# Performance work log

Measured on AMD Instinct MI355X. Metric: run time of the kernel, lower is better.

The kernel has to match this reference:

```python
import jax, jax.numpy as jnp
import numpy as np

# Fixed-shape Conformer chunked attention (Gemma3n audio style)
S = 8192          # seq_len
H = 16            # num_heads
D = 128           # head_dim
HD = H * D        # hidden size = 2048
C = 12            # chunk_size
MP = 12           # max_past_horizon
MF = 0            # max_future_horizon
CTX = C + MP + MF # context_size = 24
POS = MP + MF + 1 # pos_length = 13
N = (S + C - 1) // C            # num_blocks
PAD = N * C - S                 # pad_amount
Q_SCALE = D ** -0.5 * 1.4426950408889634  # head_dim**-0.5 / softplus(0)
SOFTCAP = 50.0


def setup_inputs() -> dict:
    key = jax.random.key(0)
    ks = jax.random.split(key, 8)
    w = lambda k, shape: jax.random.normal(k, shape, jnp.float32) * 0.02
    return {
        "hidden_states": jax.random.normal(ks[0], (1, S, HD), jnp.float32),
        "position_embeddings": jax.random.normal(ks[1], (POS, HD), jnp.float32),
        "Wq": w(ks[2], (HD, HD)),
        "Wk": w(ks[3], (HD, HD)),
        "Wv": w(ks[4], (HD, HD)),
        "W_rel": w(ks[5], (HD, HD)),
        "W_post": w(ks[6], (HD, HD)),
        "per_dim_scale": jax.random.normal(ks[7], (D,), jnp.float32) * 0.1,
    }


def reference(hidden_states, position_embeddings, Wq, Wk, Wv, W_rel, W_post, per_dim_scale):
    x = hidden_states[0]  # [S, HD]
    q = (x @ Wq).reshape(S, H, D) * (Q_SCALE * jax.nn.softplus(per_dim_scale))
    k = (x @ Wk).reshape(S, H, D)  # k_scale = 1.0
    v = (x @ Wv).reshape(S, H, D)

    # query blocks [N, C, H, D]
    qb = jnp.pad(q, ((0, PAD), (0, 0), (0, 0))).reshape(N, C, H, D)
    # key/value padded then gathered into sliding context blocks [N, CTX, H, D]
    kp = jnp.pad(k, ((MP, MF + C - 1), (0, 0), (0, 0)))
    vp = jnp.pad(v, ((MP, MF + C - 1), (0, 0), (0, 0)))
    idx = jnp.arange(N)[:, None] * C + jnp.arange(CTX)[None, :]  # [N, CTX]
    kb = kp[idx]
    vb = vp[idx]

    rel_k = (position_embeddings @ W_rel).reshape(POS, H, D)

    # content scores [H, N, C, CTX]
    ac = jnp.einsum('nchd,nkhd->hnck', qb, kb)
    # relative-position scores via shift trick
    bd = jnp.einsum('nchd,phd->hncp', qb, rel_k)          # [H, N, C, POS]
    bd = jnp.pad(bd, ((0, 0), (0, 0), (0, 0), (0, CTX + 1 - POS)))
    bd = bd.reshape(H, N, C * (CTX + 1))[:, :, :C * CTX].reshape(H, N, C, CTX)

    attn = jnp.tanh((ac + bd) / SOFTCAP) * SOFTCAP        # softcap
    attn = jax.nn.softmax(attn, axis=-1)

    out = jnp.einsum('hnck,nkhd->nchd', attn, vb).reshape(N * C, HD)[:S]
    return (out @ W_post)[None]  # [1, S, HD]
```

## Files before the change

kernel.cpp:

```cpp
#include <hip/hip_runtime.h>
#include <hip/hip_bf16.h>

#define S_LEN 8192
#define NH    16
#define HD    128
#define HID   2048
#define NQKV  6144
#define CHUNK 12
#define MP    12
#define CTX   24
#define POS   13
#define NBLK  683

typedef short bf16x8 __attribute__((ext_vector_type(8)));
typedef float f32x4  __attribute__((ext_vector_type(4)));
typedef unsigned short u16;
typedef u16 u16x8 __attribute__((ext_vector_type(8)));
typedef u16 u16x4 __attribute__((ext_vector_type(4)));

#define MFMA16 __builtin_amdgcn_mfma_f32_16x16x32_bf16

__device__ __forceinline__ void glds16(const u16* g, u16* l) {
  __builtin_amdgcn_global_load_lds(
      (__attribute__((address_space(1))) void*)(void*)g,
      (__attribute__((address_space(3))) void*)l, 16, 0, 0);
}

__device__ __forceinline__ u16 f2b(float f) {
  __hip_bfloat16 h = __float2bfloat16(f);
  return *(u16*)&h;
}

__global__ __launch_bounds__(256) void f32_to_bf16(const float* __restrict__ in,
                                                   u16* __restrict__ out, int n) {
  int i = (blockIdx.x * 256 + threadIdx.x) * 4;
  if (i < n) {
    float4 v = *(const float4*)(in + i);
    u16x4 o = {f2b(v.x), f2b(v.y), f2b(v.z), f2b(v.w)};
    *(u16x4*)(out + i) = o;
  }
}

__global__ __launch_bounds__(256) void transpose4(const float* __restrict__ W0,
                                                  const float* __restrict__ W1,
                                                  const float* __restrict__ W2,
                                                  const float* __restrict__ W3,
                                                  u16* __restrict__ out) {
  __shared__ u16 t[64][72];
  const int z = blockIdx.z;
  const float* in = (z == 0) ? W0 : (z == 1) ? W1 : (z == 2) ? W2 : W3;
  u16* dst = out + (size_t)z * HID * HID;
  const int bx = blockIdx.x * 64, by = blockIdx.y * 64;
  const int x = threadIdx.x & 63;
  const int y4 = threadIdx.x >> 6;
  for (int r = y4; r < 64; r += 4)
    t[r][x] = f2b(in[(size_t)(by + r) * HID + bx + x]);
  __syncthreads();
  for (int r = y4; r < 64; r += 4)
    dst[(size_t)(bx + r) * HID + by + x] = t[x][r];
}

__global__ void qscale_kernel(const float* __restrict__ pds, float* __restrict__ qs) {
  int d = threadIdx.x;
  float x = pds[d];
  float sp = log1pf(expf(x));
  qs[d] = 0.08838834764831845f * 1.4426950408889634f * sp;
}

__global__ __launch_bounds__(256) void relk_atomic(const float* __restrict__ pos,
                                                   const float* __restrict__ Wrel,
                                                   float* __restrict__ RELF) {
  const int col = blockIdx.x * 256 + threadIdx.x;
  const int c0 = blockIdx.y * 256;
  float acc[POS] = {};
  for (int c = c0; c < c0 + 256; ++c) {
    float wv = Wrel[(size_t)c * HID + col];
#pragma unroll
    for (int p = 0; p < POS; ++p) acc[p] += pos[p * HID + c] * wv;
  }
#pragma unroll
  for (int p = 0; p < POS; ++p) atomicAdd(&RELF[p * HID + col], acc[p]);
}

__global__ __launch_bounds__(256) void relk_cvt(const float* __restrict__ RELF,
                                                u16* __restrict__ REL) {
  int i = blockIdx.x * 256 + threadIdx.x;
  if (i < POS * HID) REL[i] = f2b(RELF[i]);
}

#define BMT 256
#define BNT 256
#define BKT 32
#define NT  (HID / BKT)

__global__ __launch_bounds__(512, 2) void gemm_bt(const u16* __restrict__ A,
                                                  const u16* __restrict__ Bt,
                                                  u16* __restrict__ Co,
                                                  float* __restrict__ Cf,
                                                  const float* __restrict__ colscale,
                                                  int NN, int csLimit) {
  __shared__ u16 lds[4][2][BMT * BKT];
  const int tid = threadIdx.x;
  const int lane = tid & 63, w = tid >> 6;
  const int quad = lane >> 4, l = lane & 15;
  const int wm = (w >> 2) * 128, wn = (w & 3) * 64;

  const int orig = blockIdx.y * gridDim.x + blockIdx.x;
  const int xcd = orig & 7, k = orig >> 3;
  const int bm = (xcd * 4 + (k & 3)) * BMT;
  const int bn = (k >> 2) * BNT;

  const int rdoff = (l >> 1) * 64 + (((((l & 1) << 2) | quad)) ^ ((l >> 1) & 7)) * 8;

  const int sl = (lane & 7) ^ (lane >> 3);
  const int srow = ((lane >> 3) << 1) + (sl >> 2);
  const int sk = (sl & 3) * 8;
  const u16* Ag0 = A + (size_t)(bm + w * 32 + srow) * HID + sk;
  const u16* Ag1 = Ag0 + (size_t)16 * HID;
  const u16* Bg0 = Bt + (size_t)(bn + w * 32 + srow) * HID + sk;
  const u16* Bg1 = Bg0 + (size_t)16 * HID;

  f32x4 acc[8][4] = {};

#pragma unroll
  for (int pt = 0; pt < 3; ++pt) {
    u16* sA = &lds[pt][0][w * 1024];
    u16* sB = &lds[pt][1][w * 1024];
    glds16(Ag0 + pt * BKT, sA);
    glds16(Ag1 + pt * BKT, sA + 512);
    glds16(Bg0 + pt * BKT, sB);
    glds16(Bg1 + pt * BKT, sB + 512);
  }
  asm volatile("s_waitcnt vmcnt(8)" ::: "memory");
  __builtin_amdgcn_s_barrier();

  bf16x8 afC[4], bfC[4], afN[4], bfN[4];
#pragma unroll
  for (int i = 0; i < 4; ++i)
    afC[i] = *(const bf16x8*)(&lds[0][0][0] + (wm + i * 16) * 32 + rdoff);
#pragma unroll
  for (int j = 0; j < 4; ++j)
    bfC[j] = *(const bf16x8*)(&lds[0][1][0] + (wn + j * 16) * 32 + rdoff);

#pragma unroll 1
  for (int t = 0; t < NT; ++t) {
    const u16* bufA = &lds[t & 3][0][0];
    u16* stA = &lds[(t + 3) & 3][0][w * 1024];
    u16* stB = &lds[(t + 3) & 3][1][w * 1024];
    const int kt = (t + 3) * BKT;
    const bool doStage = (t < NT - 3);

    if (doStage) {
      glds16(Ag0 + kt, stA);
      glds16(Ag1 + kt, stA + 512);
    }
    bf16x8 af1[4];
#pragma unroll
    for (int i = 0; i < 4; ++i)
      af1[i] = *(const bf16x8*)(bufA + (wm + 64 + i * 16) * 32 + rdoff);
    asm volatile("s_waitcnt lgkmcnt(4)" ::: "memory");
    __builtin_amdgcn_sched_barrier(0);
    __builtin_amdgcn_s_setprio(1);
#pragma unroll
    for (int i = 0; i < 4; ++i)
#pragma unroll
      for (int j = 0; j < 4; ++j)
        acc[i][j] = MFMA16(afC[i], bfC[j], acc[i][j], 0, 0, 0);
    __builtin_amdgcn_s_setprio(0);

    if (doStage) {
      glds16(Bg0 + kt, stB);
      glds16(Bg1 + kt, stB + 512);
    }
    asm volatile("s_waitcnt lgkmcnt(0)" ::: "memory");
    if (t < NT - 3)       asm volatile("s_waitcnt vmcnt(8)" ::: "memory");
    else if (t == NT - 3) asm volatile("s_waitcnt vmcnt(4)" ::: "memory");
    else if (t == NT - 2) asm volatile("s_waitcnt vmcnt(0)" ::: "memory");
    __builtin_amdgcn_sched_barrier(0);
    if (t < NT - 1) {
      __builtin_amdgcn_s_barrier();
      const u16* nA = &lds[(t + 1) & 3][0][0];
      const u16* nB = &lds[(t + 1) & 3][1][0];
#pragma unroll
      for (int i = 0; i < 4; ++i)
        afN[i] = *(const bf16x8*)(nA + (wm + i * 16) * 32 + rdoff);
#pragma unroll
      for (int j = 0; j < 4; ++j)
        bfN[j] = *(const bf16x8*)(nB + (wn + j * 16) * 32 + rdoff);
    }
    __builtin_amdgcn_s_setprio(1);
#pragma unroll
    for (int i = 0; i < 4; ++i)
#pragma unroll
      for (int j = 0; j < 4; ++j)
        acc[4 + i][j] = MFMA16(af1[i], bfC[j], acc[4 + i][j], 0, 0, 0);
    __builtin_amdgcn_s_setprio(0);
#pragma unroll
    for (int r = 0; r < 4; ++r) {
      afC[r] = afN[r];
      bfC[r] = bfN[r];
    }
  }

#pragma unroll
  for (int i = 0; i < 8; ++i)
#pragma unroll
    for (int j = 0; j < 4; ++j)
#pragma unroll
      for (int r = 0; r < 4; ++r) {
        int row = bm + wm + i * 16 + quad * 4 + r;
        int col = bn + wn + j * 16 + l;
        float v = acc[i][j][r];
        if (colscale && col < csLimit) v *= colscale[col & (HD - 1)];
        if (Cf) Cf[(size_t)row * NN + col] = v;
        else    Co[(size_t)row * NN + col] = f2b(v);
      }
}

__global__ __launch_bounds__(64) void attn_kernel(const u16* __restrict__ qkv,
                                                  const u16* __restrict__ relg,
                                                  u16* __restrict__ og) {
  __shared__ char smem[13824];
  u16* qs = (u16*)smem;
  u16* ks = (u16*)(smem + 4352);
  u16* vt = (u16*)smem;
  u16* ps = (u16*)(smem + 12288);
  const int n = blockIdx.x, h = blockIdx.y;
  const int lane = threadIdx.x;
  const int quad = lane >> 4, l = lane & 15;
  const int base = n * CHUNK;
  const u16x8 zero8 = {0, 0, 0, 0, 0, 0, 0, 0};

  const u16* qg = qkv + h * HD;
  const u16* kg = qkv + 2048 + h * HD;
  const u16* vg = qkv + 4096 + h * HD;

  u16x8 vld[8];
#pragma unroll
  for (int i = 0; i < 8; ++i) {
    int id = lane + 64 * i;
    int ctx = id & 31, dc = id >> 5;
    int s = base + ctx - MP;
    vld[i] = (ctx < CTX && s >= 0 && s < S_LEN)
                 ? *(const u16x8*)(vg + (size_t)s * NQKV + dc * 8)
                 : zero8;
  }

#pragma unroll
  for (int i = 0; i < 4; ++i) {
    int id = lane + 64 * i;
    int c = id >> 4, dc = id & 15;
    int s = base + c;
    u16x8 v = (c < CHUNK && s < S_LEN)
                  ? *(const u16x8*)(qg + (size_t)s * NQKV + dc * 8)
                  : zero8;
    *(u16x8*)(qs + c * 136 + dc * 8) = v;
  }
#pragma unroll
  for (int i = 0; i < 8; ++i) {
    int id = lane + 64 * i;
    int ctx = id >> 4, dc = id & 15;
    int s = base + ctx - MP;
    u16x8 v = (ctx < CTX && s >= 0 && s < S_LEN)
                  ? *(const u16x8*)(kg + (size_t)s * NQKV + dc * 8)
                  : zero8;
    *(u16x8*)(ks + ctx * 136 + dc * 8) = v;
  }
  __syncthreads();

  f32x4 ac0 = {0, 0, 0, 0}, ac1 = {0, 0, 0, 0}, bd = {0, 0, 0, 0};
#pragma unroll
  for (int t = 0; t < 4; ++t) {
    int d0 = t * 32;
    bf16x8 aQ = *(const bf16x8*)(qs + l * 136 + d0 + quad * 8);
    bf16x8 bK0 = *(const bf16x8*)(ks + l * 136 + d0 + quad * 8);
    bf16x8 bK1 = *(const bf16x8*)(ks + (16 + l) * 136 + d0 + quad * 8);
    bf16x8 bR = {0, 0, 0, 0, 0, 0, 0, 0};
    if (l < POS)
      bR = *(const bf16x8*)(relg + (size_t)l * HID + h * HD + d0 + quad * 8);
    ac0 = MFMA16(aQ, bK0, ac0, 0, 0, 0);
    ac1 = MFMA16(aQ, bK1, ac1, 0, 0, 0);
    bd = MFMA16(aQ, bR, bd, 0, 0, 0);
  }

  float p0[4], p1[4];
#pragma unroll
  for (int r = 0; r < 4; ++r) {
    int c = quad * 4 + r;
    int pi0 = l - c;
    int pi1 = 16 + l - c;
    int sp0 = pi0 < 0 ? 0 : (pi0 > 15 ? 15 : pi0);
    int sp1 = pi1 < 0 ? 0 : (pi1 > 15 ? 15 : pi1);
    float b0 = __shfl(bd[r], quad * 16 + sp0, 64);
    float b1 = __shfl(bd[r], quad * 16 + sp1, 64);
    b0 = (pi0 >= 0 && pi0 < POS) ? b0 : 0.0f;
    b1 = (pi1 >= 0 && pi1 < POS) ? b1 : 0.0f;
    float s0 = tanhf((ac0[r] + b0) * (1.0f / 50.0f)) * 50.0f;
    float s1 = tanhf((ac1[r] + b1) * (1.0f / 50.0f)) * 50.0f;
    bool v1 = (l < (CTX - 16));
    if (!v1) s1 = -1e30f;
    float mx = fmaxf(s0, s1);
#pragma unroll
    for (int d = 1; d < 16; d <<= 1) mx = fmaxf(mx, __shfl_xor(mx, d, 64));
    float e0 = __expf(s0 - mx);
    float e1 = v1 ? __expf(s1 - mx) : 0.0f;
    float sm = e0 + e1;
#pragma unroll
    for (int d = 1; d < 16; d <<= 1) sm += __shfl_xor(sm, d, 64);
    float inv = 1.0f / sm;
    p0[r] = e0 * inv;
    p1[r] = e1 * inv;
  }
  __syncthreads();

#pragma unroll
  for (int i = 0; i < 8; ++i) {
    int id = lane + 64 * i;
    int ctx = id & 31, dc = id >> 5;
#pragma unroll
    for (int jj = 0; jj < 8; ++jj) vt[(dc * 8 + jj) * 48 + ctx] = vld[i][jj];
  }
#pragma unroll
  for (int r = 0; r < 4; ++r) {
    int c = quad * 4 + r;
    ps[c * 48 + l] = f2b(p0[r]);
    ps[c * 48 + 16 + l] = f2b(p1[r]);
  }
  __syncthreads();

  bf16x8 aP = *(const bf16x8*)(ps + l * 48 + quad * 8);
#pragma unroll
  for (int nt = 0; nt < 8; ++nt) {
    bf16x8 bV = *(const bf16x8*)(vt + (nt * 16 + l) * 48 + quad * 8);
    f32x4 o = {0, 0, 0, 0};
    o = MFMA16(aP, bV, o, 0, 0, 0);
#pragma unroll
    for (int r = 0; r < 4; ++r) {
      int c = quad * 4 + r;
      int s = base + c;
      if (c < CHUNK && s < S_LEN)
        og[(size_t)s * HID + h * HD + nt * 16 + l] = f2b(o[r]);
    }
  }
}

extern "C" void kernel_launch(void* const* d_in, const int* in_sizes, int n_in,
                              void* d_out, int out_size, void* d_ws, size_t ws_size,
                              hipStream_t stream) {
  const float* x = (const float*)d_in[0];
  const float* pos = (const float*)d_in[1];
  const float* Wq = (const float*)d_in[2];
  const float* Wk = (const float*)d_in[3];
  const float* Wv = (const float*)d_in[4];
  const float* Wrel = (const float*)d_in[5];
  const float* Wpost = (const float*)d_in[6];
  const float* pds = (const float*)d_in[7];

  char* ws = (char*)d_ws;
  u16* WT  = (u16*)(ws);
  u16* xb  = (u16*)(ws + 33554432);
  u16* AO  = xb;
  u16* QKV = (u16*)(ws + 67108864);
  float* RELF = (float*)(ws + 167772160);
  u16* REL = (u16*)(ws + 167878656);
  float* QS = (float*)(ws + 167931904);

  const int NX = S_LEN * HID;
  f32_to_bf16<<<NX / 4 / 256, 256, 0, stream>>>(x, xb, NX);

  transpose4<<<dim3(32, 32, 4), 256, 0, stream>>>(Wq, Wk, Wv, Wpost, WT);
  qscale_kernel<<<1, 128, 0, stream>>>(pds, QS);

  hipMemsetAsync(RELF, 0, POS * HID * sizeof(float), stream);
  relk_atomic<<<dim3(8, 8), 256, 0, stream>>>(pos, Wrel, RELF);
  relk_cvt<<<(POS * HID + 255) / 256, 256, 0, stream>>>(RELF, REL);

  gemm_bt<<<dim3(32, 24), 512, 0, stream>>>(xb, WT, QKV, nullptr, QS, NQKV, 2048);

  attn_kernel<<<dim3(NBLK, NH), 64, 0, stream>>>(QKV, REL, AO);

  gemm_bt<<<dim3(32, 8), 512, 0, stream>>>(AO, WT + (size_t)3 * HID * HID,
                                           nullptr, (float*)d_out, nullptr, HID, 0);
}
```

Measured before the change: 570.6 us.

## Load Q/K MFMA fragments directly from global and swizzle V/P LDS tiles

The attention kernel no longer stages Q and K through shared memory. Each lane loads its MFMA fragments straight from global memory into registers, which removes two syncthreads and the LDS round trip. The V-transpose and P tiles are shrunk to a 32-wide stride with an XOR swizzle to avoid bank conflicts, and launch bounds now request 4 blocks per CU. The K1 rows are remapped so that lanes 0-7 of the second tile cover context 16-23, and the direct global fragment loads may coalesce less well than the old cooperative loads.

```diff
diff --git a/kernel.cpp b/kernel.cpp
--- a/kernel.cpp
+++ b/kernel.cpp
@@ -217,14 +217,11 @@
       }
 }
 
-__global__ __launch_bounds__(64) void attn_kernel(const u16* __restrict__ qkv,
-                                                  const u16* __restrict__ relg,
-                                                  u16* __restrict__ og) {
-  __shared__ char smem[13824];
-  u16* qs = (u16*)smem;
-  u16* ks = (u16*)(smem + 4352);
-  u16* vt = (u16*)smem;
-  u16* ps = (u16*)(smem + 12288);
+__global__ __launch_bounds__(64, 4) void attn_kernel(const u16* __restrict__ qkv,
+                                                     const u16* __restrict__ relg,
+                                                     u16* __restrict__ og) {
+  __shared__ u16 vt[128 * 32];
+  __shared__ u16 ps[16 * 32];
   const int n = blockIdx.x, h = blockIdx.y;
   const int lane = threadIdx.x;
   const int quad = lane >> 4, l = lane & 15;
@@ -246,41 +243,32 @@
                  : zero8;
   }
 
-#pragma unroll
-  for (int i = 0; i < 4; ++i) {
-    int id = lane + 64 * i;
-    int c = id >> 4, dc = id & 15;
-    int s = base + c;
-    u16x8 v = (c < CHUNK && s < S_LEN)
-                  ? *(const u16x8*)(qg + (size_t)s * NQKV + dc * 8)
-                  : zero8;
-    *(u16x8*)(qs + c * 136 + dc * 8) = v;
-  }
-#pragma unroll
-  for (int i = 0; i < 8; ++i) {
-    int id = lane + 64 * i;
-    int ctx = id >> 4, dc = id & 15;
-    int s = base + ctx - MP;
-    u16x8 v = (ctx < CTX && s >= 0 && s < S_LEN)
-                  ? *(const u16x8*)(kg + (size_t)s * NQKV + dc * 8)
-                  : zero8;
-    *(u16x8*)(ks + ctx * 136 + dc * 8) = v;
-  }
-  __syncthreads();
+  const bool qv = (l < CHUNK) && (base + l < S_LEN);
+  const bool k0v = (base + l - MP) >= 0;
+  const bool k1v = (l < 8) && (base + 4 + l < S_LEN);
+  const u16* qrow = qg + (size_t)(base + l) * NQKV;
+  const u16* k0row = kg + (size_t)(base + l - MP) * NQKV;
+  const u16* k1row = kg + (size_t)(base + 4 + l) * NQKV;
+
+  bf16x8 aQf[4], bK0f[4], bK1f[4];
+#pragma unroll
+  for (int t = 0; t < 4; ++t) {
+    int d0 = t * 32 + quad * 8;
+    aQf[t] = qv ? *(const bf16x8*)(qrow + d0) : (bf16x8)zero8;
+    bK0f[t] = k0v ? *(const bf16x8*)(k0row + d0) : (bf16x8)zero8;
+    bK1f[t] = k1v ? *(const bf16x8*)(k1row + d0) : (bf16x8)zero8;
+  }
 
   f32x4 ac0 = {0, 0, 0, 0}, ac1 = {0, 0, 0, 0}, bd = {0, 0, 0, 0};
 #pragma unroll
   for (int t = 0; t < 4; ++t) {
     int d0 = t * 32;
-    bf16x8 aQ = *(const bf16x8*)(qs + l * 136 + d0 + quad * 8);
-    bf16x8 bK0 = *(const bf16x8*)(ks + l * 136 + d0 + quad * 8);
-    bf16x8 bK1 = *(const bf16x8*)(ks + (16 + l) * 136 + d0 + quad * 8);
-    bf16x8 bR = {0, 0, 0, 0, 0, 0, 0, 0};
+    bf16x8 bR = (bf16x8)zero8;
     if (l < POS)
       bR = *(const bf16x8*)(relg + (size_t)l * HID + h * HD + d0 + quad * 8);
-    ac0 = MFMA16(aQ, bK0, ac0, 0, 0, 0);
-    ac1 = MFMA16(aQ, bK1, ac1, 0, 0, 0);
-    bd = MFMA16(aQ, bR, bd, 0, 0, 0);
+    ac0 = MFMA16(aQf[t], bK0f[t], ac0, 0, 0, 0);
+    ac1 = MFMA16(aQf[t], bK1f[t], ac1, 0, 0, 0);
+    bd = MFMA16(aQf[t], bR, bd, 0, 0, 0);
   }
 
   float p0[4], p1[4];
@@ -311,27 +299,33 @@
     p0[r] = e0 * inv;
     p1[r] = e1 * inv;
   }
-  __syncthreads();
 
 #pragma unroll
   for (int i = 0; i < 8; ++i) {
     int id = lane + 64 * i;
     int ctx = id & 31, dc = id >> 5;
 #pragma unroll
-    for (int jj = 0; jj < 8; ++jj) vt[(dc * 8 + jj) * 48 + ctx] = vld[i][jj];
+    for (int jj = 0; jj < 8; ++jj) {
+      int d = dc * 8 + jj;
+      int fq = (d >> 1) & 3;
+      vt[d * 32 + (((ctx >> 3) ^ fq) << 3) + (ctx & 7)] = vld[i][jj];
+    }
   }
 #pragma unroll
   for (int r = 0; r < 4; ++r) {
     int c = quad * 4 + r;
-    ps[c * 48 + l] = f2b(p0[r]);
-    ps[c * 48 + 16 + l] = f2b(p1[r]);
+    int fc = (c >> 1) & 3;
+    ps[c * 32 + (((l >> 3) ^ fc) << 3) + (l & 7)] = f2b(p0[r]);
+    ps[c * 32 + ((((16 + l) >> 3) ^ fc) << 3) + (l & 7)] = f2b(p1[r]);
   }
   __syncthreads();
 
-  bf16x8 aP = *(const bf16x8*)(ps + l * 48 + quad * 8);
+  const int fl = (l >> 1) & 3;
+  bf16x8 aP = *(const bf16x8*)(ps + l * 32 + ((quad ^ fl) << 3));
 #pragma unroll
   for (int nt = 0; nt < 8; ++nt) {
-    bf16x8 bV = *(const bf16x8*)(vt + (nt * 16 + l) * 48 + quad * 8);
+    int d = nt * 16 + l;
+    bf16x8 bV = *(const bf16x8*)(vt + d * 32 + ((quad ^ fl) << 3));
     f32x4 o = {0, 0, 0, 0};
     o = MFMA16(aP, bV, o, 0, 0, 0);
 #pragma unroll
```

Result: faster. 556.0 us (-2.6%).
